# Kernel tuning notes

Hardware: AMD Instinct MI355X
Metric: run time of the kernel (lower is better)

## Reference

```python
import jax, jax.numpy as jnp
import numpy as np

B, T, HID = 2, 4096, 1024
NH, DK, DV = 8, 128, 128
CONV_K = 4
CHUNK = 64


def short_conv_silu(x, w):
    # causal depthwise conv1d, x: [B,T,D], w: [D,K]
    K = w.shape[1]
    xp = jnp.pad(x, ((0, 0), (K - 1, 0), (0, 0)))
    out = sum(xp[:, i:i + x.shape[1], :] * w[:, i] for i in range(K))
    return jax.nn.silu(out)


def hadamard_fm(x, w1, b1, w2, b2):
    # per-head feature map: Linear(x)*Linear(x), x: [B,T,H,D]
    return (jnp.einsum('bthd,ed->bthe', x, w1) + b1) * (jnp.einsum('bthd,ed->bthe', x, w2) + b2)


def chunk_linear_attn(q, k, v, scale):
    # causal linear attention via chunked scan. q,k,v: [B,T,H,D]
    Bq, Tq, H, Dk = q.shape
    Dv = v.shape[-1]
    nc = Tq // CHUNK
    q = (q * scale).reshape(Bq, nc, CHUNK, H, Dk).transpose(1, 0, 2, 3, 4)
    k = k.reshape(Bq, nc, CHUNK, H, Dk).transpose(1, 0, 2, 3, 4)
    v = v.reshape(Bq, nc, CHUNK, H, Dv).transpose(1, 0, 2, 3, 4)
    mask = jnp.tril(jnp.ones((CHUNK, CHUNK), dtype=bool))

    def step(S, inp):
        qc, kc, vc = inp  # [B,C,H,D]
        attn = jnp.einsum('bihk,bjhk->bhij', qc, kc)
        attn = jnp.where(mask, attn, 0.0)
        o = jnp.einsum('bhij,bjhv->bihv', attn, vc) + jnp.einsum('bihk,bhkv->bihv', qc, S)
        S = S + jnp.einsum('bihk,bihv->bhkv', kc, vc)
        return S, o

    S0 = jnp.zeros((Bq, H, Dk, Dv), q.dtype)
    _, o = jax.lax.scan(step, S0, (q, k, v))  # o: [nc,B,C,H,Dv]
    return o.transpose(1, 0, 2, 3, 4).reshape(Bq, Tq, H, Dv)


def setup_inputs() -> dict:
    key = jax.random.key(0)
    ks = jax.random.split(key, 16)
    s = 0.02
    inp = {
        'hidden_states': jax.random.normal(ks[0], (B, T, HID), jnp.float32),
        'wq': jax.random.normal(ks[1], (HID, HID), jnp.float32) * s,
        'wk': jax.random.normal(ks[2], (HID, HID), jnp.float32) * s,
        'wv': jax.random.normal(ks[3], (HID, HID), jnp.float32) * s,
        'wo': jax.random.normal(ks[4], (HID, HID), jnp.float32) * s,
        'conv_q': jax.random.normal(ks[5], (HID, CONV_K), jnp.float32) * 0.2,
        'conv_k': jax.random.normal(ks[6], (HID, CONV_K), jnp.float32) * 0.2,
        'conv_v': jax.random.normal(ks[7], (HID, CONV_K), jnp.float32) * 0.2,
        'fmq_w1': jax.random.normal(ks[8], (DK, DK), jnp.float32) * s,
        'fmq_b1': jnp.zeros((DK,), jnp.float32),
        'fmq_w2': jax.random.normal(ks[9], (DK, DK), jnp.float32) * s,
        'fmq_b2': jnp.zeros((DK,), jnp.float32),
        'fmk_w1': jax.random.normal(ks[10], (DK, DK), jnp.float32) * s,
        'fmk_b1': jnp.zeros((DK,), jnp.float32),
        'fmk_w2': jax.random.normal(ks[11], (DK, DK), jnp.float32) * s,
        'fmk_b2': jnp.zeros((DK,), jnp.float32),
    }
    return inp


def reference(hidden_states, wq, wk, wv, wo, conv_q, conv_k, conv_v,
              fmq_w1, fmq_b1, fmq_w2, fmq_b2, fmk_w1, fmk_b1, fmk_w2, fmk_b2):
    q = short_conv_silu(hidden_states @ wq.T, conv_q)
    k = short_conv_silu(hidden_states @ wk.T, conv_k)
    v = short_conv_silu(hidden_states @ wv.T, conv_v)
    q = q.reshape(B, T, NH, DK)
    k = k.reshape(B, T, NH, DK)
    v = v.reshape(B, T, NH, DV)
    q = hadamard_fm(q, fmq_w1, fmq_b1, fmq_w2, fmq_b2)
    k = hadamard_fm(k, fmk_w1, fmk_b1, fmk_w2, fmk_b2)
    scale = DK ** -0.5
    o = chunk_linear_attn(q, k, v, scale)
    return o.reshape(B, T, NH * DV) @ wo.T
```

## Files before the change

### kernel.cpp

```cpp
#include <hip/hip_runtime.h>
#include <cstdint>
#include <cstddef>

#define T_SEQ 4096
#define BATCH 2
#define HIDDEN 1024
#define NHEAD 8
#define DKV 128
#define BT (BATCH * T_SEQ)
#define NCH 64
#define CHUNK_L 64
#define QSCALE 0.08838834764831845f
#define SCALE_P 1024.0f
#define SCALE_O 8192.0f
#define OEPS 0.7071067811865476f

typedef _Float16 half8 __attribute__((ext_vector_type(8)));
typedef _Float16 half4 __attribute__((ext_vector_type(4)));
typedef float floatx4 __attribute__((ext_vector_type(4)));

union HBits { _Float16 h; unsigned short u; };

__device__ __forceinline__ float silu_fast(float x)
{
    return x * __builtin_amdgcn_rcpf(1.f + __expf(-x));
}

__global__ void cast_all(const float* __restrict__ hs, _Float16* __restrict__ h16,
                         const float* __restrict__ s0, const float* __restrict__ s1,
                         const float* __restrict__ s2, const float* __restrict__ s3,
                         const float* __restrict__ s4, const float* __restrict__ s5,
                         const float* __restrict__ s6, const float* __restrict__ s7,
                         _Float16* __restrict__ d0, _Float16* __restrict__ d1,
                         _Float16* __restrict__ d2, _Float16* __restrict__ d3,
                         _Float16* __restrict__ d4, _Float16* __restrict__ d5,
                         _Float16* __restrict__ d6, _Float16* __restrict__ d7,
                         int nbig, int nsmall)
{
    if (blockIdx.y == 0) {
        int idx = blockIdx.x * 256 + threadIdx.x;
        float4 a = ((const float4*)hs)[idx * 2];
        float4 b = ((const float4*)hs)[idx * 2 + 1];
        half8 h = { (_Float16)a.x, (_Float16)a.y, (_Float16)a.z, (_Float16)a.w,
                    (_Float16)b.x, (_Float16)b.y, (_Float16)b.z, (_Float16)b.w };
        *(half8*)&h16[idx * 8] = h;
        return;
    }
    int sel = blockIdx.x >> 9;
    int inner = blockIdx.x & 511;
    const float* src; _Float16* dst; int n8;
    switch (sel) {
        case 0: src = s0; dst = d0; n8 = nbig; break;
        case 1: src = s1; dst = d1; n8 = nbig; break;
        case 2: src = s2; dst = d2; n8 = nbig; break;
        case 3: src = s3; dst = d3; n8 = nbig; break;
        case 4: src = s4; dst = d4; n8 = nsmall; break;
        case 5: src = s5; dst = d5; n8 = nsmall; break;
        case 6: src = s6; dst = d6; n8 = nsmall; break;
        default: src = s7; dst = d7; n8 = nsmall; break;
    }
    int idx = inner * 256 + threadIdx.x;
    if (idx < n8) {
        float4 u = ((const float4*)src)[idx * 2];
        float4 v = ((const float4*)src)[idx * 2 + 1];
        half8 h = { (_Float16)u.x, (_Float16)u.y, (_Float16)u.z, (_Float16)u.w,
                    (_Float16)v.x, (_Float16)v.y, (_Float16)v.z, (_Float16)v.w };
        *(half8*)&dst[idx * 8] = h;
    }
}

__global__ __launch_bounds__(256) void gemm_nt_f16_h16(const _Float16* __restrict__ A,
                                                       const _Float16* __restrict__ W,
                                                       _Float16* __restrict__ C,
                                                       int M, int N, int K, int ldc)
{
    __shared__ _Float16 As[128 * 64];
    __shared__ _Float16 Ws[128 * 64];
    const int bm = blockIdx.y * 128;
    const int bn = blockIdx.x * 128;
    const int tid = threadIdx.x;
    const int w = tid >> 6;
    const int l = tid & 63;
    const int wm = (w >> 1) * 64;
    const int wn = (w & 1) * 64;
    const int lane16 = l & 15;
    const int quad = l >> 4;
    const int srow = w * 8 + (l >> 3);
    const int skh = ((l & 7) ^ (l >> 3)) * 8;
    const int rsw = lane16 & 7;

    floatx4 acc[4][4];
#pragma unroll
    for (int i = 0; i < 4; ++i)
#pragma unroll
        for (int j = 0; j < 4; ++j)
            acc[i][j] = (floatx4){0.f, 0.f, 0.f, 0.f};

    for (int k0 = 0; k0 < K; k0 += 64) {
#pragma unroll
        for (int c = 0; c < 4; ++c) {
            int row = c * 32 + srow;
            const _Float16* ga = A + (size_t)(bm + row) * K + k0 + skh;
            const _Float16* gw = W + (size_t)(bn + row) * K + k0 + skh;
            __builtin_amdgcn_global_load_lds(
                (const __attribute__((address_space(1))) void*)ga,
                (__attribute__((address_space(3))) void*)(As + c * 2048 + w * 512), 16, 0, 0);
            __builtin_amdgcn_global_load_lds(
                (const __attribute__((address_space(1))) void*)gw,
                (__attribute__((address_space(3))) void*)(Ws + c * 2048 + w * 512), 16, 0, 0);
        }
        __syncthreads();

#pragma unroll
        for (int s = 0; s < 2; ++s) {
            const int pc = (((s * 4 + quad) ^ rsw)) * 8;
            half8 a[4], b[4];
#pragma unroll
            for (int i = 0; i < 4; ++i) {
                a[i] = *(const half8*)&As[(wm + i * 16 + lane16) * 64 + pc];
                b[i] = *(const half8*)&Ws[(wn + i * 16 + lane16) * 64 + pc];
            }
#pragma unroll
            for (int i = 0; i < 4; ++i)
#pragma unroll
                for (int j = 0; j < 4; ++j)
                    acc[i][j] = __builtin_amdgcn_mfma_f32_16x16x32_f16(a[i], b[j], acc[i][j], 0, 0, 0);
        }
        __syncthreads();
    }
#pragma unroll
    for (int i = 0; i < 4; ++i)
#pragma unroll
        for (int j = 0; j < 4; ++j)
#pragma unroll
            for (int r = 0; r < 4; ++r)
                C[(size_t)(bm + wm + i * 16 + quad * 4 + r) * ldc + bn + wn + j * 16 + lane16] =
                    (_Float16)acc[i][j][r];
}

__global__ __launch_bounds__(256) void gemm_nt_f16_f32(const _Float16* __restrict__ A,
                                                       const _Float16* __restrict__ W,
                                                       float* __restrict__ C,
                                                       int M, int N, int K, float scale)
{
    __shared__ _Float16 As[128 * 64];
    __shared__ _Float16 Ws[128 * 64];
    const int bm = blockIdx.y * 128;
    const int bn = blockIdx.x * 128;
    const int tid = threadIdx.x;
    const int w = tid >> 6;
    const int l = tid & 63;
    const int wm = (w >> 1) * 64;
    const int wn = (w & 1) * 64;
    const int lane16 = l & 15;
    const int quad = l >> 4;
    const int srow = w * 8 + (l >> 3);
    const int skh = ((l & 7) ^ (l >> 3)) * 8;
    const int rsw = lane16 & 7;

    floatx4 acc[4][4];
#pragma unroll
    for (int i = 0; i < 4; ++i)
#pragma unroll
        for (int j = 0; j < 4; ++j)
            acc[i][j] = (floatx4){0.f, 0.f, 0.f, 0.f};

    for (int k0 = 0; k0 < K; k0 += 64) {
#pragma unroll
        for (int c = 0; c < 4; ++c) {
            int row = c * 32 + srow;
            const _Float16* ga = A + (size_t)(bm + row) * K + k0 + skh;
            const _Float16* gw = W + (size_t)(bn + row) * K + k0 + skh;
            __builtin_amdgcn_global_load_lds(
                (const __attribute__((address_space(1))) void*)ga,
                (__attribute__((address_space(3))) void*)(As + c * 2048 + w * 512), 16, 0, 0);
            __builtin_amdgcn_global_load_lds(
                (const __attribute__((address_space(1))) void*)gw,
                (__attribute__((address_space(3))) void*)(Ws + c * 2048 + w * 512), 16, 0, 0);
        }
        __syncthreads();

#pragma unroll
        for (int s = 0; s < 2; ++s) {
            const int pc = (((s * 4 + quad) ^ rsw)) * 8;
            half8 a[4], b[4];
#pragma unroll
            for (int i = 0; i < 4; ++i) {
                a[i] = *(const half8*)&As[(wm + i * 16 + lane16) * 64 + pc];
                b[i] = *(const half8*)&Ws[(wn + i * 16 + lane16) * 64 + pc];
            }
#pragma unroll
            for (int i = 0; i < 4; ++i)
#pragma unroll
                for (int j = 0; j < 4; ++j)
                    acc[i][j] = __builtin_amdgcn_mfma_f32_16x16x32_f16(a[i], b[j], acc[i][j], 0, 0, 0);
        }
        __syncthreads();
    }
#pragma unroll
    for (int i = 0; i < 4; ++i)
#pragma unroll
        for (int j = 0; j < 4; ++j)
#pragma unroll
            for (int r = 0; r < 4; ++r)
                C[(size_t)(bm + wm + i * 16 + quad * 4 + r) * N + bn + wn + j * 16 + lane16] =
                    acc[i][j][r] * scale;
}

#define XIN_LD 136
#define XS_LD 40
#define XS_SLAB (64 * XS_LD)
#define OS_LD 72
#define SMEM_HALFS (67 * XIN_LD + 4 * XS_SLAB)

__global__ __launch_bounds__(256) void conv_all(const _Float16* __restrict__ QKV, int ldx,
                                                const float* __restrict__ Wcq,
                                                const float* __restrict__ Wck,
                                                const float* __restrict__ Wcv,
                                                const _Float16* __restrict__ Wfm,
                                                const float* __restrict__ Bq1,
                                                const float* __restrict__ Bq2,
                                                const float* __restrict__ Bk1,
                                                const float* __restrict__ Bk2,
                                                _Float16* __restrict__ OUTq,
                                                _Float16* __restrict__ OUTk,
                                                _Float16* __restrict__ VT)
{
    __shared__ __align__(16) _Float16 smem[SMEM_HALFS];
    const int zsel = blockIdx.z;
    const int tid = threadIdx.x;

    if (zsel >= 2) {
        _Float16* xs = smem;
        _Float16* os = smem + 4288;
        const int bx = (zsel - 2) * 1024 + blockIdx.y * 128 + blockIdx.x;
        const int t0 = (bx & 63) * 64;
        const int dt = ((bx >> 6) & 15) * 64;
        const int z = bx >> 10;

#pragma unroll
        for (int i = 0; i < 3; ++i) {
            int p = tid + 256 * i;
            if (p < 536) {
                int row = p >> 3, d8 = (p & 7) * 8;
                int t = t0 - 3 + row;
                half8 v;
                if (t >= 0)
                    v = *(const half8*)&QKV[((size_t)z * T_SEQ + t) * ldx + 2 * HIDDEN + dt + d8];
                else
                    v = (half8){0, 0, 0, 0, 0, 0, 0, 0};
                *(half8*)&xs[row * 64 + d8] = v;
            }
        }
        __syncthreads();

        const int d = tid & 63;
        float4 w = *(const float4*)&Wcv[(dt + d) * 4];
#pragma unroll
        for (int u = 0; u < 2; ++u) {
            int tg = (tid >> 6) + u * 4;
            half8 o;
#pragma unroll
            for (int s = 0; s < 8; ++s) {
                int base = (tg * 8 + s + 3) * 64 + d;
                float acc = (float)xs[base] * w.w
                          + (float)xs[base - 64] * w.z
                          + (float)xs[base - 128] * w.y
                          + (float)xs[base - 192] * w.x;
                o[s] = (_Float16)silu_fast(acc);
            }
            *(half8*)&os[d * OS_LD + tg * 8] = o;
        }
        __syncthreads();

#pragma unroll
        for (int u = 0; u < 2; ++u) {
            int p = tid + u * 256;
            int row = p >> 3, ch = p & 7;
            half8 v = *(const half8*)&os[row * OS_LD + ch * 8];
            *(half8*)&VT[((size_t)z * HIDDEN + dt + row) * T_SEQ + t0 + ch * 8] = v;
        }
        return;
    }

    const int sel = zsel;
    const float* Wc = sel ? Wck : Wcq;
    const _Float16* W1h = Wfm + (sel ? 2 * 16384 : 0);
    const _Float16* W2h = Wfm + (sel ? 3 * 16384 : 16384);
    const float* B1 = sel ? Bk1 : Bq1;
    const float* B2 = sel ? Bk2 : Bq2;
    _Float16* OUT = sel ? OUTk : OUTq;

    _Float16* xin = smem;
    _Float16* xs = smem + 67 * XIN_LD;
    const int t0 = blockIdx.x * 64;
    const int h = blockIdx.y;
    const int w = tid >> 6;
    const int l = tid & 63;
    const int lane16 = l & 15;
    const int quad = l >> 4;
    const bool batch_start = (t0 & (T_SEQ - 1)) == 0;
    const int ebase = w * 32 + lane16;

    half8 pb1[2], pb2[2];
    float b1v[2], b2v[2];
#pragma unroll
    for (int nt = 0; nt < 2; ++nt) {
        pb1[nt] = *(const half8*)&W1h[(size_t)(ebase + nt * 16) * DKV + quad * 8];
        pb2[nt] = *(const half8*)&W2h[(size_t)(ebase + nt * 16) * DKV + quad * 8];
        b1v[nt] = B1[ebase + nt * 16];
        b2v[nt] = B2[ebase + nt * 16];
    }

    for (int p = tid; p < 67 * 16; p += 256) {
        int row = p >> 4, cg = p & 15;
        half8 v;
        if (batch_start && row < 3)
            v = (half8){0, 0, 0, 0, 0, 0, 0, 0};
        else
            v = *(const half8*)&QKV[(size_t)(t0 - 3 + row) * ldx + sel * HIDDEN + h * DKV + cg * 8];
        *(half8*)&xin[row * XIN_LD + cg * 8] = v;
    }
    __syncthreads();

    {
        const int doct = tid & 15;
        const int d0 = doct * 8;
        const int rq = (tid >> 4) * 4;
        const int u = doct >> 2;
        const int col = d0 & 31;

        float w0[8], w1[8], w2[8], w3[8];
#pragma unroll
        for (int e = 0; e < 8; ++e) {
            float4 wv = *(const float4*)&Wc[(h * DKV + d0 + e) * 4];
            w0[e] = wv.x; w1[e] = wv.y; w2[e] = wv.z; w3[e] = wv.w;
        }

#pragma unroll
        for (int rr = 0; rr < 4; ++rr) {
            const int row = rq + rr;
            half8 x3 = *(const half8*)&xin[(row + 0) * XIN_LD + d0];
            half8 x2 = *(const half8*)&xin[(row + 1) * XIN_LD + d0];
            half8 x1 = *(const half8*)&xin[(row + 2) * XIN_LD + d0];
            half8 x0 = *(const half8*)&xin[(row + 3) * XIN_LD + d0];
            half8 o;
#pragma unroll
            for (int e = 0; e < 8; ++e) {
                float acc = fmaf((float)x0[e], w3[e],
                            fmaf((float)x1[e], w2[e],
                            fmaf((float)x2[e], w1[e], (float)x3[e] * w0[e])));
                o[e] = (_Float16)silu_fast(acc);
            }
            *(half8*)&xs[u * XS_SLAB + row * XS_LD + col] = o;
        }
    }
    __syncthreads();

    floatx4 acc1[4][2], acc2[4][2];
#pragma unroll
    for (int i = 0; i < 4; ++i)
#pragma unroll
        for (int j = 0; j < 2; ++j) {
            acc1[i][j] = (floatx4){0.f, 0.f, 0.f, 0.f};
            acc2[i][j] = (floatx4){0.f, 0.f, 0.f, 0.f};
        }

#pragma unroll
    for (int s = 0; s < 4; ++s) {
        half8 nb1[2], nb2[2];
        if (s < 3) {
#pragma unroll
            for (int nt = 0; nt < 2; ++nt) {
                nb1[nt] = *(const half8*)&W1h[(size_t)(ebase + nt * 16) * DKV + (s + 1) * 32 + quad * 8];
                nb2[nt] = *(const half8*)&W2h[(size_t)(ebase + nt * 16) * DKV + (s + 1) * 32 + quad * 8];
            }
        }
        half8 a[4];
#pragma unroll
        for (int mt = 0; mt < 4; ++mt)
            a[mt] = *(const half8*)&xs[s * XS_SLAB + (mt * 16 + lane16) * XS_LD + quad * 8];
#pragma unroll
        for (int nt = 0; nt < 2; ++nt) {
#pragma unroll
            for (int mt = 0; mt < 4; ++mt) {
                acc1[mt][nt] = __builtin_amdgcn_mfma_f32_16x16x32_f16(a[mt], pb1[nt], acc1[mt][nt], 0, 0, 0);
                acc2[mt][nt] = __builtin_amdgcn_mfma_f32_16x16x32_f16(a[mt], pb2[nt], acc2[mt][nt], 0, 0, 0);
            }
        }
        if (s < 3) {
            pb1[0] = nb1[0]; pb1[1] = nb1[1];
            pb2[0] = nb2[0]; pb2[1] = nb2[1];
        }
    }

#pragma unroll
    for (int nt = 0; nt < 2; ++nt) {
#pragma unroll
        for (int mt = 0; mt < 4; ++mt)
#pragma unroll
            for (int r = 0; r < 4; ++r) {
                float o = (acc1[mt][nt][r] + b1v[nt]) * (acc2[mt][nt][r] + b2v[nt]);
                OUT[(size_t)(t0 + mt * 16 + quad * 4 + r) * HIDDEN + h * DKV + ebase + nt * 16] = (_Float16)o;
            }
    }
}

__global__ __launch_bounds__(256) void ktv_mfma(const _Float16* __restrict__ Kf,
                                                const _Float16* __restrict__ VT,
                                                _Float16* __restrict__ G16)
{
    __shared__ _Float16 kt[128 * 72];
    const int c = blockIdx.x;
    const int bh = blockIdx.y;
    const int b = bh >> 3, h = bh & 7;
    const int tid = threadIdx.x;
    const int w = tid >> 6;
    const int l = tid & 63;
    const int lane16 = l & 15;
    const int quad = l >> 4;
    const size_t rowbase = (size_t)b * T_SEQ + (size_t)c * CHUNK_L;

    const int m0 = (w >> 1) * 64;
    const int n0 = (w & 1) * 64;
    half8 vta[2][4];
#pragma unroll
    for (int s = 0; s < 2; ++s)
#pragma unroll
        for (int mt = 0; mt < 4; ++mt) {
            int dv = m0 + mt * 16 + lane16;
            vta[s][mt] = *(const half8*)&VT[((size_t)bh * DKV + dv) * T_SEQ + c * CHUNK_L + s * 32 + quad * 8];
        }

    {
        const int dk0 = (tid >> 4) * 8;
        const int jb = (tid & 15) * 4;
        half8 r0 = *(const half8*)&Kf[(rowbase + jb + 0) * HIDDEN + h * DKV + dk0];
        half8 r1 = *(const half8*)&Kf[(rowbase + jb + 1) * HIDDEN + h * DKV + dk0];
        half8 r2 = *(const half8*)&Kf[(rowbase + jb + 2) * HIDDEN + h * DKV + dk0];
        half8 r3 = *(const half8*)&Kf[(rowbase + jb + 3) * HIDDEN + h * DKV + dk0];
#pragma unroll
        for (int dk = 0; dk < 8; ++dk) {
            HBits a0, a1, a2, a3;
            a0.h = r0[dk]; a1.h = r1[dk]; a2.h = r2[dk]; a3.h = r3[dk];
            unsigned int lo = ((unsigned int)a1.u << 16) | a0.u;
            unsigned int hi = ((unsigned int)a3.u << 16) | a2.u;
            *(unsigned int*)&kt[(dk0 + dk) * 72 + jb] = lo;
            *(unsigned int*)&kt[(dk0 + dk) * 72 + jb + 2] = hi;
        }
    }
    __syncthreads();

    floatx4 acc[4][4];
#pragma unroll
    for (int i = 0; i < 4; ++i)
#pragma unroll
        for (int j = 0; j < 4; ++j)
            acc[i][j] = (floatx4){0.f, 0.f, 0.f, 0.f};

#pragma unroll
    for (int s = 0; s < 2; ++s) {
        half8 bb[4];
#pragma unroll
        for (int nt = 0; nt < 4; ++nt)
            bb[nt] = *(const half8*)&kt[(n0 + nt * 16 + lane16) * 72 + s * 32 + quad * 8];
#pragma unroll
        for (int mt = 0; mt < 4; ++mt)
#pragma unroll
            for (int nt = 0; nt < 4; ++nt)
                acc[mt][nt] = __builtin_amdgcn_mfma_f32_16x16x32_f16(vta[s][mt], bb[nt], acc[mt][nt], 0, 0, 0);
    }

    _Float16* Gp = G16 + ((size_t)bh * NCH + c) * (DKV * DKV);
#pragma unroll
    for (int mt = 0; mt < 4; ++mt)
#pragma unroll
        for (int nt = 0; nt < 4; ++nt)
#pragma unroll
            for (int r = 0; r < 4; ++r)
                Gp[(size_t)(m0 + mt * 16 + quad * 4 + r) * DKV + n0 + nt * 16 + lane16] =
                    (_Float16)acc[mt][nt][r];
}

__global__ void prefix_kernel(const _Float16* __restrict__ G16, _Float16* __restrict__ Gh)
{
    int idx = blockIdx.x * 256 + threadIdx.x;
    int bh = idx >> 12;
    int e4 = (idx & 4095) * 4;
    const _Float16* p = G16 + (size_t)bh * NCH * 16384 + e4;
    _Float16* q = Gh + (size_t)bh * NCH * 16384 + e4;
    float r0 = 0.f, r1 = 0.f, r2 = 0.f, r3 = 0.f;
#pragma unroll 8
    for (int c = 0; c < NCH; ++c) {
        half4 g = *(const half4*)&p[(size_t)c * 16384];
        half4 o = { (_Float16)(r0 * SCALE_P), (_Float16)(r1 * SCALE_P),
                    (_Float16)(r2 * SCALE_P), (_Float16)(r3 * SCALE_P) };
        *(half4*)&q[(size_t)c * 16384] = o;
        r0 += (float)g[0]; r1 += (float)g[1]; r2 += (float)g[2]; r3 += (float)g[3];
    }
}

#define PSLD 40
__global__ __launch_bounds__(256) void attn_mfma(const _Float16* __restrict__ Qf,
                                                 const _Float16* __restrict__ Kf,
                                                 const _Float16* __restrict__ VT,
                                                 const _Float16* __restrict__ Gh,
                                                 _Float16* __restrict__ O)
{
    __shared__ _Float16 ps[2 * 64 * PSLD];
    const int c = blockIdx.x;
    const int bh = blockIdx.y;
    const int b = bh >> 3, h = bh & 7;
    const int tid = threadIdx.x;
    const int w = tid >> 6;
    const int l = tid & 63;
    const int lane16 = l & 15;
    const int quad = l >> 4;
    const size_t rowbase = (size_t)b * T_SEQ + (size_t)c * CHUNK_L;
    const int n0o = w * 32;
    const _Float16* gh = Gh + ((size_t)bh * NCH + c) * (DKV * DKV);

    half8 vtpre[2][2];
#pragma unroll
    for (int s = 0; s < 2; ++s)
#pragma unroll
        for (int nt = 0; nt < 2; ++nt) {
            int dv = n0o + nt * 16 + lane16;
            vtpre[s][nt] = *(const half8*)&VT[((size_t)bh * DKV + dv) * T_SEQ + c * CHUNK_L + s * 32 + quad * 8];
        }
    half8 ghp[2];
#pragma unroll
    for (int nt = 0; nt < 2; ++nt)
        ghp[nt] = *(const half8*)&gh[(size_t)(n0o + nt * 16 + lane16) * DKV + quad * 8];

    {
        const int m0 = (w >> 1) * 32;
        const int n0 = (w & 1) * 32;
        floatx4 aq[2][2];
#pragma unroll
        for (int i = 0; i < 2; ++i)
#pragma unroll
            for (int j = 0; j < 2; ++j)
                aq[i][j] = (floatx4){0.f, 0.f, 0.f, 0.f};
#pragma unroll
        for (int s = 0; s < 4; ++s) {
            half8 a[2], bb[2];
#pragma unroll
            for (int mt = 0; mt < 2; ++mt)
                a[mt] = *(const half8*)&Qf[(rowbase + m0 + mt * 16 + lane16) * HIDDEN +
                                           h * DKV + s * 32 + quad * 8];
#pragma unroll
            for (int nt = 0; nt < 2; ++nt)
                bb[nt] = *(const half8*)&Kf[(rowbase + n0 + nt * 16 + lane16) * HIDDEN +
                                            h * DKV + s * 32 + quad * 8];
#pragma unroll
            for (int mt = 0; mt < 2; ++mt)
#pragma unroll
                for (int nt = 0; nt < 2; ++nt)
                    aq[mt][nt] = __builtin_amdgcn_mfma_f32_16x16x32_f16(a[mt], bb[nt], aq[mt][nt], 0, 0, 0);
        }
#pragma unroll
        for (int mt = 0; mt < 2; ++mt)
#pragma unroll
            for (int nt = 0; nt < 2; ++nt) {
                int j = n0 + nt * 16 + lane16;
#pragma unroll
                for (int r = 0; r < 4; ++r) {
                    int i = m0 + mt * 16 + quad * 4 + r;
                    float v = (j <= i) ? aq[mt][nt][r] * SCALE_P : 0.f;
                    ps[(j >> 5) * 64 * PSLD + i * PSLD + (j & 31)] = (_Float16)v;
                }
            }
    }
    __syncthreads();

    floatx4 accO[4][2];
#pragma unroll
    for (int i = 0; i < 4; ++i)
#pragma unroll
        for (int j = 0; j < 2; ++j)
            accO[i][j] = (floatx4){0.f, 0.f, 0.f, 0.f};

#pragma unroll
    for (int s = 0; s < 2; ++s) {
        half8 a[4];
#pragma unroll
        for (int mt = 0; mt < 4; ++mt)
            a[mt] = *(const half8*)&ps[s * 64 * PSLD + (mt * 16 + lane16) * PSLD + quad * 8];
#pragma unroll
        for (int mt = 0; mt < 4; ++mt)
#pragma unroll
            for (int nt = 0; nt < 2; ++nt)
                accO[mt][nt] = __builtin_amdgcn_mfma_f32_16x16x32_f16(a[mt], vtpre[s][nt], accO[mt][nt], 0, 0, 0);
    }

#pragma unroll
    for (int s = 0; s < 4; ++s) {
        half8 nb[2];
        if (s < 3) {
#pragma unroll
            for (int nt = 0; nt < 2; ++nt)
                nb[nt] = *(const half8*)&gh[(size_t)(n0o + nt * 16 + lane16) * DKV + (s + 1) * 32 + quad * 8];
        }
        half8 a[4];
#pragma unroll
        for (int mt = 0; mt < 4; ++mt)
            a[mt] = *(const half8*)&Qf[(rowbase + mt * 16 + lane16) * HIDDEN +
                                       h * DKV + s * 32 + quad * 8];
#pragma unroll
        for (int mt = 0; mt < 4; ++mt)
#pragma unroll
            for (int nt = 0; nt < 2; ++nt)
                accO[mt][nt] = __builtin_amdgcn_mfma_f32_16x16x32_f16(a[mt], ghp[nt], accO[mt][nt], 0, 0, 0);
        if (s < 3) { ghp[0] = nb[0]; ghp[1] = nb[1]; }
    }

#pragma unroll
    for (int mt = 0; mt < 4; ++mt)
#pragma unroll
        for (int nt = 0; nt < 2; ++nt)
#pragma unroll
            for (int r = 0; r < 4; ++r)
                O[(rowbase + mt * 16 + quad * 4 + r) * HIDDEN + h * DKV + n0o + nt * 16 + lane16] =
                    (_Float16)(accO[mt][nt][r] * OEPS);
}

extern "C" void kernel_launch(void* const* d_in, const int* in_sizes, int n_in,
                              void* d_out, int out_size, void* d_ws, size_t ws_size,
                              hipStream_t stream)
{
    (void)in_sizes; (void)n_in; (void)out_size; (void)ws_size;
    const float* hs = (const float*)d_in[0];
    const float* wq = (const float*)d_in[1];
    const float* wk = (const float*)d_in[2];
    const float* wv = (const float*)d_in[3];
    const float* wo = (const float*)d_in[4];
    const float* cq = (const float*)d_in[5];
    const float* ck = (const float*)d_in[6];
    const float* cv = (const float*)d_in[7];
    const float* fmq_w1 = (const float*)d_in[8];
    const float* fmq_b1 = (const float*)d_in[9];
    const float* fmq_w2 = (const float*)d_in[10];
    const float* fmq_b2 = (const float*)d_in[11];
    const float* fmk_w1 = (const float*)d_in[12];
    const float* fmk_b1 = (const float*)d_in[13];
    const float* fmk_w2 = (const float*)d_in[14];
    const float* fmk_b2 = (const float*)d_in[15];
    float* out = (float*)d_out;
    char* ws = (char*)d_ws;

    const size_t MB = 1024 * 1024;
    _Float16* h16     = (_Float16*)(ws + 0);
    _Float16* qf16    = (_Float16*)(ws + 0);
    _Float16* wqkv16  = (_Float16*)(ws + 16 * MB);
    _Float16* wo16    = wqkv16 + (3 << 20);
    _Float16* fmw     = wqkv16 + (4 << 20);
    _Float16* qkvlin  = (_Float16*)(ws + 32 * MB);
    _Float16* kf16    = (_Float16*)(ws + 80 * MB);
    _Float16* vT      = (_Float16*)(ws + 96 * MB);
    _Float16* O16     = (_Float16*)(ws + 112 * MB);
    _Float16* G16     = (_Float16*)(ws + 128 * MB);
    _Float16* Gh      = (_Float16*)(ws + 160 * MB);

    cast_all<<<dim3(4096, 2), 256, 0, stream>>>(
        hs, h16,
        wq, wk, wv, wo, fmq_w1, fmq_w2, fmk_w1, fmk_w2,
        wqkv16, wqkv16 + (1 << 20), wqkv16 + (2 << 20), wo16,
        fmw, fmw + 16384, fmw + 2 * 16384, fmw + 3 * 16384,
        HIDDEN * HIDDEN / 8, DKV * DKV / 8);

    dim3 gqkv(3 * HIDDEN / 128, BT / 128);
    gemm_nt_f16_h16<<<gqkv, 256, 0, stream>>>(h16, wqkv16, qkvlin,
                                              BT, 3 * HIDDEN, HIDDEN, 3 * HIDDEN);

    dim3 cg(BT / 64, NHEAD, 4);
    conv_all<<<cg, 256, 0, stream>>>(qkvlin, 3 * HIDDEN, cq, ck, cv, fmw,
                                     fmq_b1, fmq_b2, fmk_b1, fmk_b2,
                                     qf16, kf16, vT);

    dim3 ag(NCH, BATCH * NHEAD);
    ktv_mfma<<<ag, 256, 0, stream>>>(kf16, vT, G16);
    prefix_kernel<<<256, 256, 0, stream>>>(G16, Gh);
    attn_mfma<<<ag, 256, 0, stream>>>(qf16, kf16, vT, Gh, O16);

    dim3 gg(HIDDEN / 128, BT / 128);
    gemm_nt_f16_f32<<<gg, 256, 0, stream>>>(O16, wo16, out, BT, HIDDEN, HIDDEN, 1.0f / SCALE_O);
}
```

Before: 304.9 us.

## Fuse K^T V chunk-state GEMM and V conv into the K feature-map kernel

Merges the value conv/transposition and the per-chunk K^T V product into the conv/feature-map kernel. Blocks that compute K keep the feature-mapped K tile in shared memory, then convolve V, transpose it in LDS and run the MFMA chunk GEMM without reloading K or V from global memory. This removes one kernel launch and the global round trip of kf16/vT for ktv. In exchange, the grid becomes unbalanced because K blocks do much more work than Q blocks, and shared-memory use per block rises.

Result: slower. 315.6 us (+3.5%).

```diff
diff --git a/kernel.cpp b/kernel.cpp
--- a/kernel.cpp
+++ b/kernel.cpp
@@ -210,80 +210,41 @@
 #define XIN_LD 136
 #define XS_LD 40
 #define XS_SLAB (64 * XS_LD)
-#define OS_LD 72
-#define SMEM_HALFS (67 * XIN_LD + 4 * XS_SLAB)
-
-__global__ __launch_bounds__(256) void conv_all(const _Float16* __restrict__ QKV, int ldx,
-                                                const float* __restrict__ Wcq,
-                                                const float* __restrict__ Wck,
-                                                const float* __restrict__ Wcv,
-                                                const _Float16* __restrict__ Wfm,
-                                                const float* __restrict__ Bq1,
-                                                const float* __restrict__ Bq2,
-                                                const float* __restrict__ Bk1,
-                                                const float* __restrict__ Bk2,
-                                                _Float16* __restrict__ OUTq,
-                                                _Float16* __restrict__ OUTk,
-                                                _Float16* __restrict__ VT)
-{
-    __shared__ __align__(16) _Float16 smem[SMEM_HALFS];
-    const int zsel = blockIdx.z;
+#define KT_LD 72
+#define BUF1_HALFS 9216
+#define BUF2_HALFS 10240
+
+__global__ __launch_bounds__(256) void conv_fused(const _Float16* __restrict__ QKV, int ldx,
+                                                  const float* __restrict__ Wcq,
+                                                  const float* __restrict__ Wck,
+                                                  const float* __restrict__ Wcv,
+                                                  const _Float16* __restrict__ Wfm,
+                                                  const float* __restrict__ Bq1,
+                                                  const float* __restrict__ Bq2,
+                                                  const float* __restrict__ Bk1,
+                                                  const float* __restrict__ Bk2,
+                                                  _Float16* __restrict__ OUTq,
+                                                  _Float16* __restrict__ OUTk,
+                                                  _Float16* __restrict__ VT,
+                                                  _Float16* __restrict__ G16)
+{
+    __shared__ __align__(16) _Float16 buf1[BUF1_HALFS];
+    __shared__ __align__(16) _Float16 buf2[BUF2_HALFS];
+    const int kind = blockIdx.x & 1;
+    const int xx = blockIdx.x >> 1;
+    const int bh = blockIdx.y;
     const int tid = threadIdx.x;
-
-    if (zsel >= 2) {
-        _Float16* xs = smem;
-        _Float16* os = smem + 4288;
-        const int bx = (zsel - 2) * 1024 + blockIdx.y * 128 + blockIdx.x;
-        const int t0 = (bx & 63) * 64;
-        const int dt = ((bx >> 6) & 15) * 64;
-        const int z = bx >> 10;
-
-#pragma unroll
-        for (int i = 0; i < 3; ++i) {
-            int p = tid + 256 * i;
-            if (p < 536) {
-                int row = p >> 3, d8 = (p & 7) * 8;
-                int t = t0 - 3 + row;
-                half8 v;
-                if (t >= 0)
-                    v = *(const half8*)&QKV[((size_t)z * T_SEQ + t) * ldx + 2 * HIDDEN + dt + d8];
-                else
-                    v = (half8){0, 0, 0, 0, 0, 0, 0, 0};
-                *(half8*)&xs[row * 64 + d8] = v;
-            }
-        }
-        __syncthreads();
-
-        const int d = tid & 63;
-        float4 w = *(const float4*)&Wcv[(dt + d) * 4];
-#pragma unroll
-        for (int u = 0; u < 2; ++u) {
-            int tg = (tid >> 6) + u * 4;
-            half8 o;
-#pragma unroll
-            for (int s = 0; s < 8; ++s) {
-                int base = (tg * 8 + s + 3) * 64 + d;
-                float acc = (float)xs[base] * w.w
-                          + (float)xs[base - 64] * w.z
-                          + (float)xs[base - 128] * w.y
-                          + (float)xs[base - 192] * w.x;
-                o[s] = (_Float16)silu_fast(acc);
-            }
-            *(half8*)&os[d * OS_LD + tg * 8] = o;
-        }
-        __syncthreads();
-
-#pragma unroll
-        for (int u = 0; u < 2; ++u) {
-            int p = tid + u * 256;
-            int row = p >> 3, ch = p & 7;
-            half8 v = *(const half8*)&os[row * OS_LD + ch * 8];
-            *(half8*)&VT[((size_t)z * HIDDEN + dt + row) * T_SEQ + t0 + ch * 8] = v;
-        }
-        return;
-    }
-
-    const int sel = zsel;
+    const int w = tid >> 6;
+    const int l = tid & 63;
+    const int lane16 = l & 15;
+    const int quad = l >> 4;
+    const int ebase = w * 32 + lane16;
+
+    const int sel = kind ? 0 : 1;
+    const int h = bh & 7;
+    const int t0 = kind ? ((bh >> 3) * 64 + xx) * 64
+                        : (((bh >> 3) * 64 + xx) * 64);
+    const bool batch_start = (xx == 0);
     const float* Wc = sel ? Wck : Wcq;
     const _Float16* W1h = Wfm + (sel ? 2 * 16384 : 0);
     const _Float16* W2h = Wfm + (sel ? 3 * 16384 : 16384);
@@ -291,17 +252,6 @@
     const float* B2 = sel ? Bk2 : Bq2;
     _Float16* OUT = sel ? OUTk : OUTq;
 
-    _Float16* xin = smem;
-    _Float16* xs = smem + 67 * XIN_LD;
-    const int t0 = blockIdx.x * 64;
-    const int h = blockIdx.y;
-    const int w = tid >> 6;
-    const int l = tid & 63;
-    const int lane16 = l & 15;
-    const int quad = l >> 4;
-    const bool batch_start = (t0 & (T_SEQ - 1)) == 0;
-    const int ebase = w * 32 + lane16;
-
     half8 pb1[2], pb2[2];
     float b1v[2], b2v[2];
 #pragma unroll
@@ -311,6 +261,9 @@
         b1v[nt] = B1[ebase + nt * 16];
         b2v[nt] = B2[ebase + nt * 16];
     }
+
+    _Float16* xin = buf1;
+    _Float16* xs = buf2;
 
     for (int p = tid; p < 67 * 16; p += 256) {
         int row = p >> 4, cg = p & 15;
@@ -323,20 +276,18 @@
     }
     __syncthreads();
 
+    const int doct = tid & 15;
+    const int d0 = doct * 8;
+    const int rq = (tid >> 4) * 4;
     {
-        const int doct = tid & 15;
-        const int d0 = doct * 8;
-        const int rq = (tid >> 4) * 4;
         const int u = doct >> 2;
         const int col = d0 & 31;
-
         float w0[8], w1[8], w2[8], w3[8];
 #pragma unroll
         for (int e = 0; e < 8; ++e) {
             float4 wv = *(const float4*)&Wc[(h * DKV + d0 + e) * 4];
             w0[e] = wv.x; w1[e] = wv.y; w2[e] = wv.z; w3[e] = wv.w;
         }
-
 #pragma unroll
         for (int rr = 0; rr < 4; ++rr) {
             const int row = rq + rr;
@@ -365,7 +316,6 @@
             acc1[i][j] = (floatx4){0.f, 0.f, 0.f, 0.f};
             acc2[i][j] = (floatx4){0.f, 0.f, 0.f, 0.f};
         }
-
 #pragma unroll
     for (int s = 0; s < 4; ++s) {
         half8 nb1[2], nb2[2];
@@ -394,63 +344,94 @@
         }
     }
 
+    _Float16* kt = buf1;
 #pragma unroll
     for (int nt = 0; nt < 2; ++nt) {
-#pragma unroll
-        for (int mt = 0; mt < 4; ++mt)
+        const int e = ebase + nt * 16;
+#pragma unroll
+        for (int mt = 0; mt < 4; ++mt) {
+            HBits hb[4];
 #pragma unroll
             for (int r = 0; r < 4; ++r) {
                 float o = (acc1[mt][nt][r] + b1v[nt]) * (acc2[mt][nt][r] + b2v[nt]);
-                OUT[(size_t)(t0 + mt * 16 + quad * 4 + r) * HIDDEN + h * DKV + ebase + nt * 16] = (_Float16)o;
-            }
-    }
-}
-
-__global__ __launch_bounds__(256) void ktv_mfma(const _Float16* __restrict__ Kf,
-                                                const _Float16* __restrict__ VT,
-                                                _Float16* __restrict__ G16)
-{
-    __shared__ _Float16 kt[128 * 72];
-    const int c = blockIdx.x;
-    const int bh = blockIdx.y;
-    const int b = bh >> 3, h = bh & 7;
-    const int tid = threadIdx.x;
-    const int w = tid >> 6;
-    const int l = tid & 63;
-    const int lane16 = l & 15;
-    const int quad = l >> 4;
-    const size_t rowbase = (size_t)b * T_SEQ + (size_t)c * CHUNK_L;
+                hb[r].h = (_Float16)o;
+                OUT[(size_t)(t0 + mt * 16 + quad * 4 + r) * HIDDEN + h * DKV + e] = hb[r].h;
+            }
+            if (kind == 0) {
+                const int j0 = mt * 16 + quad * 4;
+                unsigned int lo = ((unsigned int)hb[1].u << 16) | hb[0].u;
+                unsigned int hi = ((unsigned int)hb[3].u << 16) | hb[2].u;
+                *(unsigned int*)&kt[e * KT_LD + j0] = lo;
+                *(unsigned int*)&kt[e * KT_LD + j0 + 2] = hi;
+            }
+        }
+    }
+
+    if (kind == 1) return;
+
+    const int c = xx;
+    __syncthreads();
+
+    _Float16* vwin = buf2;
+    for (int p = tid; p < 67 * 16; p += 256) {
+        int row = p >> 4, cg = p & 15;
+        half8 v;
+        if (batch_start && row < 3)
+            v = (half8){0, 0, 0, 0, 0, 0, 0, 0};
+        else
+            v = *(const half8*)&QKV[(size_t)(t0 - 3 + row) * ldx + 2 * HIDDEN + h * DKV + cg * 8];
+        *(half8*)&vwin[row * XIN_LD + cg * 8] = v;
+    }
+    __syncthreads();
+
+    half8 ov[4];
+    {
+        float4 wv[8];
+#pragma unroll
+        for (int e = 0; e < 8; ++e)
+            wv[e] = *(const float4*)&Wcv[(h * DKV + d0 + e) * 4];
+#pragma unroll
+        for (int rr = 0; rr < 4; ++rr) {
+            const int row = rq + rr;
+            half8 x3 = *(const half8*)&vwin[(row + 0) * XIN_LD + d0];
+            half8 x2 = *(const half8*)&vwin[(row + 1) * XIN_LD + d0];
+            half8 x1 = *(const half8*)&vwin[(row + 2) * XIN_LD + d0];
+            half8 x0 = *(const half8*)&vwin[(row + 3) * XIN_LD + d0];
+#pragma unroll
+            for (int e = 0; e < 8; ++e) {
+                float acc = (float)x0[e] * wv[e].w
+                          + (float)x1[e] * wv[e].z
+                          + (float)x2[e] * wv[e].y
+                          + (float)x3[e] * wv[e].x;
+                ov[rr][e] = (_Float16)silu_fast(acc);
+            }
+        }
+    }
+    __syncthreads();
+
+    _Float16* vt = buf2;
+#pragma unroll
+    for (int ee = 0; ee < 8; ++ee) {
+        const int e = (ee + doct) & 7;
+        HBits a0, a1, a2, a3;
+        a0.h = ov[0][e]; a1.h = ov[1][e]; a2.h = ov[2][e]; a3.h = ov[3][e];
+        unsigned int lo = ((unsigned int)a1.u << 16) | a0.u;
+        unsigned int hi = ((unsigned int)a3.u << 16) | a2.u;
+        *(unsigned int*)&vt[(d0 + e) * KT_LD + rq] = lo;
+        *(unsigned int*)&vt[(d0 + e) * KT_LD + rq + 2] = hi;
+    }
+    __syncthreads();
+
+#pragma unroll
+    for (int u = 0; u < 4; ++u) {
+        int p = tid + u * 256;
+        int row = p >> 3, ch = p & 7;
+        half8 v = *(const half8*)&vt[row * KT_LD + ch * 8];
+        *(half8*)&VT[((size_t)bh * DKV + row) * T_SEQ + c * CHUNK_L + ch * 8] = v;
+    }
 
     const int m0 = (w >> 1) * 64;
     const int n0 = (w & 1) * 64;
-    half8 vta[2][4];
-#pragma unroll
-    for (int s = 0; s < 2; ++s)
-#pragma unroll
-        for (int mt = 0; mt < 4; ++mt) {
-            int dv = m0 + mt * 16 + lane16;
-            vta[s][mt] = *(const half8*)&VT[((size_t)bh * DKV + dv) * T_SEQ + c * CHUNK_L + s * 32 + quad * 8];
-        }
-
-    {
-        const int dk0 = (tid >> 4) * 8;
-        const int jb = (tid & 15) * 4;
-        half8 r0 = *(const half8*)&Kf[(rowbase + jb + 0) * HIDDEN + h * DKV + dk0];
-        half8 r1 = *(const half8*)&Kf[(rowbase + jb + 1) * HIDDEN + h * DKV + dk0];
-        half8 r2 = *(const half8*)&Kf[(rowbase + jb + 2) * HIDDEN + h * DKV + dk0];
-        half8 r3 = *(const half8*)&Kf[(rowbase + jb + 3) * HIDDEN + h * DKV + dk0];
-#pragma unroll
-        for (int dk = 0; dk < 8; ++dk) {
-            HBits a0, a1, a2, a3;
-            a0.h = r0[dk]; a1.h = r1[dk]; a2.h = r2[dk]; a3.h = r3[dk];
-            unsigned int lo = ((unsigned int)a1.u << 16) | a0.u;
-            unsigned int hi = ((unsigned int)a3.u << 16) | a2.u;
-            *(unsigned int*)&kt[(dk0 + dk) * 72 + jb] = lo;
-            *(unsigned int*)&kt[(dk0 + dk) * 72 + jb + 2] = hi;
-        }
-    }
-    __syncthreads();
-
     floatx4 acc[4][4];
 #pragma unroll
     for (int i = 0; i < 4; ++i)
@@ -460,15 +441,18 @@
 
 #pragma unroll
     for (int s = 0; s < 2; ++s) {
-        half8 bb[4];
+        half8 a[4], bb[4];
+#pragma unroll
+        for (int mt = 0; mt < 4; ++mt)
+            a[mt] = *(const half8*)&vt[(m0 + mt * 16 + lane16) * KT_LD + s * 32 + quad * 8];
 #pragma unroll
         for (int nt = 0; nt < 4; ++nt)
-            bb[nt] = *(const half8*)&kt[(n0 + nt * 16 + lane16) * 72 + s * 32 + quad * 8];
+            bb[nt] = *(const half8*)&kt[(n0 + nt * 16 + lane16) * KT_LD + s * 32 + quad * 8];
 #pragma unroll
         for (int mt = 0; mt < 4; ++mt)
 #pragma unroll
             for (int nt = 0; nt < 4; ++nt)
-                acc[mt][nt] = __builtin_amdgcn_mfma_f32_16x16x32_f16(vta[s][mt], bb[nt], acc[mt][nt], 0, 0, 0);
+                acc[mt][nt] = __builtin_amdgcn_mfma_f32_16x16x32_f16(a[mt], bb[nt], acc[mt][nt], 0, 0, 0);
     }
 
     _Float16* Gp = G16 + ((size_t)bh * NCH + c) * (DKV * DKV);
@@ -673,14 +657,13 @@
     gemm_nt_f16_h16<<<gqkv, 256, 0, stream>>>(h16, wqkv16, qkvlin,
                                               BT, 3 * HIDDEN, HIDDEN, 3 * HIDDEN);
 
-    dim3 cg(BT / 64, NHEAD, 4);
-    conv_all<<<cg, 256, 0, stream>>>(qkvlin, 3 * HIDDEN, cq, ck, cv, fmw,
-                                     fmq_b1, fmq_b2, fmk_b1, fmk_b2,
-                                     qf16, kf16, vT);
-
+    dim3 cg(128, 16);
+    conv_fused<<<cg, 256, 0, stream>>>(qkvlin, 3 * HIDDEN, cq, ck, cv, fmw,
+                                       fmq_b1, fmq_b2, fmk_b1, fmk_b2,
+                                       qf16, kf16, vT, G16);
+
+    prefix_kernel<<<256, 256, 0, stream>>>(G16, Gh);
     dim3 ag(NCH, BATCH * NHEAD);
-    ktv_mfma<<<ag, 256, 0, stream>>>(kf16, vT, G16);
-    prefix_kernel<<<256, 256, 0, stream>>>(G16, Gh);
     attn_mfma<<<ag, 256, 0, stream>>>(qf16, kf16, vT, Gh, O16);
 
     dim3 gg(HIDDEN / 128, BT / 128);
```
